# Optimization experiments

Measured on AMD Instinct MI355X. Metric: run time of the kernel, lower is better.

## Reference

```python
import jax, jax.numpy as jnp
import numpy as np
from math import pi

B, CIN, COUT, H, W, K, STRIDE, PAD = 4, 32, 64, 32, 32, 3, 1, 1


def setup_inputs() -> dict:
    key = jax.random.key(0)
    k1, k2, k3 = jax.random.split(key, 3)
    x = jax.random.normal(k1, (B, CIN, H, W), dtype=jnp.float32)
    probe = jax.random.uniform(k2, (1, CIN, COUT, 1, 1, K, K), dtype=jnp.float32, minval=-pi, maxval=pi)
    out_w = jax.random.uniform(k3, (1, CIN, COUT, 1, 1, K, K), dtype=jnp.float32, minval=-pi, maxval=pi)
    return {"x": x, "probe": probe, "out_w": out_w}


def _patches(x):
    # sliding-window gather, equivalent to x.unfold(2,K,S).unfold(3,K,S)
    p = jax.lax.conv_general_dilated_patches(
        x, filter_shape=(K, K), window_strides=(STRIDE, STRIDE),
        padding=[(PAD, PAD), (PAD, PAD)])  # (B, CIN*K*K, Ho, Wo), channel-major
    b, _, ho, wo = p.shape
    p = p.reshape(b, CIN, K, K, ho, wo)
    return jnp.transpose(p, (0, 1, 4, 5, 2, 3))  # (B, CIN, Ho, Wo, K, K)


def reference(x, probe, out_w):
    pat = _patches(x)[:, :, None]                 # (B, CIN, 1, Ho, Wo, K, K)
    act = jnp.cos(pat - probe) ** 3               # (B, CIN, COUT, Ho, Wo, K, K)
    cw = jnp.cos(out_w).reshape(CIN, COUT, K, K)  # squeeze broadcast dims
    sw = jnp.sin(out_w).reshape(CIN, COUT, K, K)
    out_x = jnp.einsum('cokl,bcohwkl->bohw', cw, act)
    out_y = jnp.einsum('cokl,bcohwkl->bohw', sw, act)
    return jnp.arctan2(out_y, out_x)              # (B, COUT, Ho, Wo)
```

## Files before the change

kernel.cpp:

```cpp
#include <hip/hip_runtime.h>
#include <math.h>


typedef _Float16 half8 __attribute__((ext_vector_type(8)));
typedef _Float16 half4 __attribute__((ext_vector_type(4)));
typedef float floatx4 __attribute__((ext_vector_type(4)));

#define B_TAP_STRIDE (16 * 128 * 16)
#define B_VSTRIDE (9u * 16 * 128 * 16)
#define FLAG_OFF (1u << 20)

#define AL_OFF 26112

#define BLOAD(dst, base)                     \
  do {                                       \
    dst##0 = *(const half8*)((base));        \
    dst##1 = *(const half8*)((base) + 8192); \
    dst##2 = *(const half8*)((base) + 16384);\
    dst##3 = *(const half8*)((base) + 24576);\
  } while (0)

__global__ __launch_bounds__(512, 2) void ring_fused(
    const float* __restrict__ x, const float* __restrict__ probe,
    const float* __restrict__ outw, char* __restrict__ Bg,
    float* __restrict__ out) {
  __shared__ __align__(16) char sA[52224];
  __shared__ float sEx[1024];

  int blk = blockIdx.x;
  int oh = blk & 1;
  int h = (blk >> 1) & 31;
  int b = blk >> 6;
  int tid = threadIdx.x;

  if (tid < 72) {
    int i = blk * 72 + tid;
    int q = i & 15;
    int n = (i >> 4) & 127;
    int tap = i >> 11;
    int o = n & 63;
    int xy = n >> 6;
    half8 hi, lo;
#pragma unroll
    for (int hf = 0; hf < 2; ++hf) {
      int c = q * 2 + hf;
      int idx = (c * 64 + o) * 9 + tap;
      float th = probe[idx];
      float wvv = outw[idx];
      float sth, cth, sw, cw;
      __sincosf(th, &sth, &cth);
      __sincosf(wvv, &sw, &cw);
      float c3 = cth * fmaf(4.0f * cth, cth, -3.0f);
      float s3 = sth * fmaf(-4.0f * sth, sth, 3.0f);
      float m = xy ? sw : cw;
      float v4[4] = {0.75f * m * cth, 0.75f * m * sth, 0.25f * m * c3,
                     0.25f * m * s3};
#pragma unroll
      for (int f = 0; f < 4; ++f) {
        _Float16 hv = (_Float16)v4[f];
        hi[hf * 4 + f] = hv;
        lo[hf * 4 + f] = (_Float16)((v4[f] - (float)hv) * 2048.0f);
      }
    }
    size_t off = (((size_t)tap * 16 + q) * 128 + n) * 16;
    *(half8*)(Bg + off) = hi;
    *(half8*)(Bg + off + B_VSTRIDE) = lo;
  }

  int lane = tid & 63;
  int wv = tid >> 6;
  int n16 = lane & 15;
  int quad = lane >> 4;
  int wt = wv >> 2;
  int xy = (wv >> 1) & 1;
  int og = wv & 1;

  {
    float xv[7];
#pragma unroll
    for (int it = 0; it < 7; ++it) {
      int u = tid + it * 512;
      int colidx = u % 34;
      int t = u / 34;
      int c = t & 31;
      int r = t >> 5;
      int hs = h + r - 1;
      int wsx = colidx - 1;
      bool valid = (u < 3264) && ((unsigned)hs < 32u) && ((unsigned)wsx < 32u);
      int xi = ((b * 32 + c) * 32 + ((unsigned)hs < 32u ? hs : 0)) * 32 +
               ((unsigned)wsx < 32u ? wsx : 0);
      xv[it] = valid ? x[xi] : 0.0f;
    }
#pragma unroll
    for (int it = 0; it < 7; ++it) {
      int u = tid + it * 512;
      if (u < 3264) {
        int colidx = u % 34;
        int t = u / 34;
        int c = t & 31;
        int r = t >> 5;
        int q = c >> 1;
        int hf = c & 1;
        int p = q ^ (colidx & 7);
        float s1, c1;
        __sincosf(xv[it], &s1, &c1);
        float c3 = c1 * fmaf(4.0f * c1, c1, -3.0f);
        float s3 = s1 * fmaf(-4.0f * s1, s1, 3.0f);
        float v4[4] = {c1, s1, c3, s3};
        half4 hi4, lo4;
#pragma unroll
        for (int f = 0; f < 4; ++f) {
          _Float16 hv = (_Float16)v4[f];
          hi4[f] = hv;
          lo4[f] = (_Float16)((v4[f] - (float)hv) * 2048.0f);
        }
        int ub = ((r * 34 + colidx) * 16 + p) * 16 + hf * 8;
        *(half4*)(sA + ub) = hi4;
        *(half4*)(sA + ub + AL_OFF) = lo4;
      }
    }
  }

  __syncthreads();
  unsigned int* flag = (unsigned int*)(Bg + FLAG_OFF);
  if (tid == 0) {
    __threadfence();
    atomicAdd(flag, 1u);
    while (atomicAdd(flag, 0u) < 256u) {
      __builtin_amdgcn_s_sleep(8);
    }
    __threadfence();
  }
  __syncthreads();

  int n_global = xy * 64 + oh * 32 + og * 16 + n16;
  const char* bLane = Bg + quad * 2048 + (size_t)n_global * 16;

  half8 BcH0, BcH1, BcH2, BcH3, BcL0, BcL1, BcL2, BcL3;
  half8 BnH0, BnH1, BnH2, BnH3, BnL0, BnL1, BnL2, BnL3;
  half8 BtH0, BtH1, BtH2, BtH3, BtL0, BtL1, BtL2, BtL3;
  BLOAD(BcH, bLane);
  BLOAD(BcL, bLane + B_VSTRIDE);
  BLOAD(BnH, bLane + B_TAP_STRIDE);
  BLOAD(BnL, bLane + B_TAP_STRIDE + B_VSTRIDE);

  floatx4 acc0 = {0.f, 0.f, 0.f, 0.f};
  floatx4 acc1 = {0.f, 0.f, 0.f, 0.f};
  floatx4 acc2 = {0.f, 0.f, 0.f, 0.f};

#pragma unroll
  for (int tap = 0; tap < 9; ++tap) {
    if (tap < 7) {
      const char* bt = bLane + (size_t)(tap + 2) * B_TAP_STRIDE;
      BLOAD(BtH, bt);
      BLOAD(BtL, bt + B_VSTRIDE);
    }

    int dk = tap / 3;
    int l = tap - dk * 3;
    int colidx = wt * 16 + n16 + l;
    int akey = colidx & 7;
    const char* aH = sA + (dk * 34 + colidx) * 256;
    const char* aL = aH + AL_OFF;

#pragma unroll
    for (int ks = 0; ks < 4; ++ks) {
      int pa = ((ks * 4 + quad) ^ akey) * 16;
      half8 Ah = *(const half8*)(aH + pa);
      half8 Al = *(const half8*)(aL + pa);
      half8 Bh = (ks == 0) ? BcH0 : (ks == 1) ? BcH1 : (ks == 2) ? BcH2 : BcH3;
      half8 Bl = (ks == 0) ? BcL0 : (ks == 1) ? BcL1 : (ks == 2) ? BcL2 : BcL3;
      acc0 = __builtin_amdgcn_mfma_f32_16x16x32_f16(Ah, Bh, acc0, 0, 0, 0);
      acc1 = __builtin_amdgcn_mfma_f32_16x16x32_f16(Al, Bh, acc1, 0, 0, 0);
      acc2 = __builtin_amdgcn_mfma_f32_16x16x32_f16(Ah, Bl, acc2, 0, 0, 0);
    }
    BcH0 = BnH0; BcH1 = BnH1; BcH2 = BnH2; BcH3 = BnH3;
    BcL0 = BnL0; BcL1 = BnL1; BcL2 = BnL2; BcL3 = BnL3;
    BnH0 = BtH0; BnH1 = BtH1; BnH2 = BtH2; BnH3 = BtH3;
    BnL0 = BtL0; BnL1 = BtL1; BnL2 = BtL2; BnL3 = BtL3;
  }

  floatx4 fin = acc0 + (acc1 + acc2) * (1.0f / 2048.0f);

  __syncthreads();
  if (xy == 1) {
#pragma unroll
    for (int r = 0; r < 4; ++r)
      sEx[((wt * 2 + og) * 16 + n16) * 16 + quad * 4 + r] = fin[r];
  }
  __syncthreads();
  if (xy == 0) {
    int o = oh * 32 + og * 16 + n16;
    float4 res;
    float* rp = (float*)&res;
#pragma unroll
    for (int r = 0; r < 4; ++r) {
      int m = quad * 4 + r;
      float ay = sEx[((wt * 2 + og) * 16 + n16) * 16 + m];
      rp[r] = atan2f(ay, fin[r]);
    }
    float* dst = out + (((size_t)(b * 64 + o) * 32 + h) * 32 + wt * 16 + quad * 4);
    *(float4*)dst = res;
  }
}

extern "C" void kernel_launch(void* const* d_in, const int* in_sizes, int n_in,
                              void* d_out, int out_size, void* d_ws, size_t ws_size,
                              hipStream_t stream) {
  const float* x = (const float*)d_in[0];
  const float* probe = (const float*)d_in[1];
  const float* outw = (const float*)d_in[2];
  char* Bg = (char*)d_ws;
  float* out = (float*)d_out;

  hipMemsetAsync(Bg + FLAG_OFF, 0, 4, stream);
  ring_fused<<<256, 512, 0, stream>>>(x, probe, outw, Bg, out);
}
```

Baseline: 80.06 us.

## Split weight prep into separate kernel and split K across waves

The weight-table preparation moves out of the fused kernel into its own small kernel, so the grid-wide atomic spin barrier and the flag memset go away. The main kernel now gives each wave half the channel chunks for both column tiles instead of all channels for one tile. Partial sums are reduced through shared memory before atan2. B-fragment register pressure is halved, so B loads can be issued before the A staging, but there is an extra launch and a heavier LDS reduction.

```diff
diff --git a/kernel.cpp b/kernel.cpp
--- a/kernel.cpp
+++ b/kernel.cpp
@@ -8,24 +8,56 @@
 
 #define B_TAP_STRIDE (16 * 128 * 16)
 #define B_VSTRIDE (9u * 16 * 128 * 16)
-#define FLAG_OFF (1u << 20)
 
 #define AL_OFF 26112
 
-#define BLOAD(dst, base)                     \
+__global__ __launch_bounds__(256) void ring_prep_b(
+    const float* __restrict__ probe, const float* __restrict__ outw,
+    char* __restrict__ Bg) {
+  int i = blockIdx.x * 256 + threadIdx.x;
+  int q = i & 15;
+  int n = (i >> 4) & 127;
+  int tap = i >> 11;
+  int o = n & 63;
+  int xy = n >> 6;
+  half8 hi, lo;
+#pragma unroll
+  for (int hf = 0; hf < 2; ++hf) {
+    int c = q * 2 + hf;
+    int idx = (c * 64 + o) * 9 + tap;
+    float th = probe[idx];
+    float wvv = outw[idx];
+    float sth, cth, sw, cw;
+    __sincosf(th, &sth, &cth);
+    __sincosf(wvv, &sw, &cw);
+    float c3 = cth * fmaf(4.0f * cth, cth, -3.0f);
+    float s3 = sth * fmaf(-4.0f * sth, sth, 3.0f);
+    float m = xy ? sw : cw;
+    float v4[4] = {0.75f * m * cth, 0.75f * m * sth, 0.25f * m * c3,
+                   0.25f * m * s3};
+#pragma unroll
+    for (int f = 0; f < 4; ++f) {
+      _Float16 hv = (_Float16)v4[f];
+      hi[hf * 4 + f] = hv;
+      lo[hf * 4 + f] = (_Float16)((v4[f] - (float)hv) * 2048.0f);
+    }
+  }
+  size_t off = (((size_t)tap * 16 + q) * 128 + n) * 16;
+  *(half8*)(Bg + off) = hi;
+  *(half8*)(Bg + off + B_VSTRIDE) = lo;
+}
+
+#define BLOAD2(dst, base)                    \
   do {                                       \
     dst##0 = *(const half8*)((base));        \
     dst##1 = *(const half8*)((base) + 8192); \
-    dst##2 = *(const half8*)((base) + 16384);\
-    dst##3 = *(const half8*)((base) + 24576);\
   } while (0)
 
-__global__ __launch_bounds__(512, 2) void ring_fused(
-    const float* __restrict__ x, const float* __restrict__ probe,
-    const float* __restrict__ outw, char* __restrict__ Bg,
+__global__ __launch_bounds__(512, 2) void ring_mfma(
+    const float* __restrict__ x, const char* __restrict__ Bg,
     float* __restrict__ out) {
   __shared__ __align__(16) char sA[52224];
-  __shared__ float sEx[1024];
+  __shared__ __align__(16) float sR[4096];
 
   int blk = blockIdx.x;
   int oh = blk & 1;
@@ -33,47 +65,24 @@
   int b = blk >> 6;
   int tid = threadIdx.x;
 
-  if (tid < 72) {
-    int i = blk * 72 + tid;
-    int q = i & 15;
-    int n = (i >> 4) & 127;
-    int tap = i >> 11;
-    int o = n & 63;
-    int xy = n >> 6;
-    half8 hi, lo;
-#pragma unroll
-    for (int hf = 0; hf < 2; ++hf) {
-      int c = q * 2 + hf;
-      int idx = (c * 64 + o) * 9 + tap;
-      float th = probe[idx];
-      float wvv = outw[idx];
-      float sth, cth, sw, cw;
-      __sincosf(th, &sth, &cth);
-      __sincosf(wvv, &sw, &cw);
-      float c3 = cth * fmaf(4.0f * cth, cth, -3.0f);
-      float s3 = sth * fmaf(-4.0f * sth, sth, 3.0f);
-      float m = xy ? sw : cw;
-      float v4[4] = {0.75f * m * cth, 0.75f * m * sth, 0.25f * m * c3,
-                     0.25f * m * s3};
-#pragma unroll
-      for (int f = 0; f < 4; ++f) {
-        _Float16 hv = (_Float16)v4[f];
-        hi[hf * 4 + f] = hv;
-        lo[hf * 4 + f] = (_Float16)((v4[f] - (float)hv) * 2048.0f);
-      }
-    }
-    size_t off = (((size_t)tap * 16 + q) * 128 + n) * 16;
-    *(half8*)(Bg + off) = hi;
-    *(half8*)(Bg + off + B_VSTRIDE) = lo;
-  }
-
   int lane = tid & 63;
   int wv = tid >> 6;
   int n16 = lane & 15;
   int quad = lane >> 4;
-  int wt = wv >> 2;
+  int kg = wv >> 2;
   int xy = (wv >> 1) & 1;
   int og = wv & 1;
+
+  int n_global = xy * 64 + oh * 32 + og * 16 + n16;
+  const char* bLane = Bg + (kg * 8 + quad) * 2048 + (size_t)n_global * 16;
+
+  half8 BcH0, BcH1, BcL0, BcL1;
+  half8 BnH0, BnH1, BnL0, BnL1;
+  half8 BtH0, BtH1, BtL0, BtL1;
+  BLOAD2(BcH, bLane);
+  BLOAD2(BcL, bLane + B_VSTRIDE);
+  BLOAD2(BnH, bLane + B_TAP_STRIDE);
+  BLOAD2(BnL, bLane + B_TAP_STRIDE + B_VSTRIDE);
 
   {
     float xv[7];
@@ -121,86 +130,77 @@
     }
   }
 
+  floatx4 acc0[2], acc1[2], acc2[2];
+#pragma unroll
+  for (int wt = 0; wt < 2; ++wt) {
+    acc0[wt] = (floatx4){0.f, 0.f, 0.f, 0.f};
+    acc1[wt] = (floatx4){0.f, 0.f, 0.f, 0.f};
+    acc2[wt] = (floatx4){0.f, 0.f, 0.f, 0.f};
+  }
+
   __syncthreads();
-  unsigned int* flag = (unsigned int*)(Bg + FLAG_OFF);
-  if (tid == 0) {
-    __threadfence();
-    atomicAdd(flag, 1u);
-    while (atomicAdd(flag, 0u) < 256u) {
-      __builtin_amdgcn_s_sleep(8);
-    }
-    __threadfence();
-  }
-  __syncthreads();
-
-  int n_global = xy * 64 + oh * 32 + og * 16 + n16;
-  const char* bLane = Bg + quad * 2048 + (size_t)n_global * 16;
-
-  half8 BcH0, BcH1, BcH2, BcH3, BcL0, BcL1, BcL2, BcL3;
-  half8 BnH0, BnH1, BnH2, BnH3, BnL0, BnL1, BnL2, BnL3;
-  half8 BtH0, BtH1, BtH2, BtH3, BtL0, BtL1, BtL2, BtL3;
-  BLOAD(BcH, bLane);
-  BLOAD(BcL, bLane + B_VSTRIDE);
-  BLOAD(BnH, bLane + B_TAP_STRIDE);
-  BLOAD(BnL, bLane + B_TAP_STRIDE + B_VSTRIDE);
-
-  floatx4 acc0 = {0.f, 0.f, 0.f, 0.f};
-  floatx4 acc1 = {0.f, 0.f, 0.f, 0.f};
-  floatx4 acc2 = {0.f, 0.f, 0.f, 0.f};
 
 #pragma unroll
   for (int tap = 0; tap < 9; ++tap) {
     if (tap < 7) {
       const char* bt = bLane + (size_t)(tap + 2) * B_TAP_STRIDE;
-      BLOAD(BtH, bt);
-      BLOAD(BtL, bt + B_VSTRIDE);
+      BLOAD2(BtH, bt);
+      BLOAD2(BtL, bt + B_VSTRIDE);
     }
 
     int dk = tap / 3;
     int l = tap - dk * 3;
-    int colidx = wt * 16 + n16 + l;
-    int akey = colidx & 7;
-    const char* aH = sA + (dk * 34 + colidx) * 256;
-    const char* aL = aH + AL_OFF;
-
-#pragma unroll
-    for (int ks = 0; ks < 4; ++ks) {
-      int pa = ((ks * 4 + quad) ^ akey) * 16;
-      half8 Ah = *(const half8*)(aH + pa);
-      half8 Al = *(const half8*)(aL + pa);
-      half8 Bh = (ks == 0) ? BcH0 : (ks == 1) ? BcH1 : (ks == 2) ? BcH2 : BcH3;
-      half8 Bl = (ks == 0) ? BcL0 : (ks == 1) ? BcL1 : (ks == 2) ? BcL2 : BcL3;
-      acc0 = __builtin_amdgcn_mfma_f32_16x16x32_f16(Ah, Bh, acc0, 0, 0, 0);
-      acc1 = __builtin_amdgcn_mfma_f32_16x16x32_f16(Al, Bh, acc1, 0, 0, 0);
-      acc2 = __builtin_amdgcn_mfma_f32_16x16x32_f16(Ah, Bl, acc2, 0, 0, 0);
-    }
-    BcH0 = BnH0; BcH1 = BnH1; BcH2 = BnH2; BcH3 = BnH3;
-    BcL0 = BnL0; BcL1 = BnL1; BcL2 = BnL2; BcL3 = BnL3;
-    BnH0 = BtH0; BnH1 = BtH1; BnH2 = BtH2; BnH3 = BtH3;
-    BnL0 = BtL0; BnL1 = BtL1; BnL2 = BtL2; BnL3 = BtL3;
-  }
-
-  floatx4 fin = acc0 + (acc1 + acc2) * (1.0f / 2048.0f);
-
+#pragma unroll
+    for (int wt = 0; wt < 2; ++wt) {
+      int colidx = wt * 16 + n16 + l;
+      int akey = colidx & 7;
+      const char* aH = sA + (dk * 34 + colidx) * 256;
+      const char* aL = aH + AL_OFF;
+#pragma unroll
+      for (int ksl = 0; ksl < 2; ++ksl) {
+        int chunk = (kg * 2 + ksl) * 4 + quad;
+        int pa = (chunk ^ akey) * 16;
+        half8 Ah = *(const half8*)(aH + pa);
+        half8 Al = *(const half8*)(aL + pa);
+        half8 Bh = ksl ? BcH1 : BcH0;
+        half8 Bl = ksl ? BcL1 : BcL0;
+        acc0[wt] = __builtin_amdgcn_mfma_f32_16x16x32_f16(Ah, Bh, acc0[wt], 0, 0, 0);
+        acc1[wt] = __builtin_amdgcn_mfma_f32_16x16x32_f16(Al, Bh, acc1[wt], 0, 0, 0);
+        acc2[wt] = __builtin_amdgcn_mfma_f32_16x16x32_f16(Ah, Bl, acc2[wt], 0, 0, 0);
+      }
+    }
+    BcH0 = BnH0; BcH1 = BnH1; BcL0 = BnL0; BcL1 = BnL1;
+    BnH0 = BtH0; BnH1 = BtH1; BnL0 = BtL0; BnL1 = BtL1;
+  }
+
+  floatx4 finA = acc0[0] + (acc1[0] + acc2[0]) * (1.0f / 2048.0f);
+  floatx4 finB = acc0[1] + (acc1[1] + acc2[1]) * (1.0f / 2048.0f);
+
+  if (wv >= 2) {
+    int basei = wv * 512 + n16 * 16 + quad * 4;
+    *(floatx4*)(sR + basei) = finA;
+    *(floatx4*)(sR + basei + 256) = finB;
+  }
   __syncthreads();
-  if (xy == 1) {
-#pragma unroll
-    for (int r = 0; r < 4; ++r)
-      sEx[((wt * 2 + og) * 16 + n16) * 16 + quad * 4 + r] = fin[r];
-  }
-  __syncthreads();
-  if (xy == 0) {
+  if (wv < 2) {
     int o = oh * 32 + og * 16 + n16;
-    float4 res;
-    float* rp = (float*)&res;
-#pragma unroll
-    for (int r = 0; r < 4; ++r) {
-      int m = quad * 4 + r;
-      float ay = sEx[((wt * 2 + og) * 16 + n16) * 16 + m];
-      rp[r] = atan2f(ay, fin[r]);
-    }
-    float* dst = out + (((size_t)(b * 64 + o) * 32 + h) * 32 + wt * 16 + quad * 4);
-    *(float4*)dst = res;
+#pragma unroll
+    for (int wt = 0; wt < 2; ++wt) {
+      floatx4 fin = wt ? finB : finA;
+      int sb = wt * 256 + n16 * 16 + quad * 4;
+      floatx4 axE = *(const floatx4*)(sR + (4 + og) * 512 + sb);
+      floatx4 ay1 = *(const floatx4*)(sR + (2 + og) * 512 + sb);
+      floatx4 ay2 = *(const floatx4*)(sR + (6 + og) * 512 + sb);
+      floatx4 ax4 = fin + axE;
+      floatx4 ay4 = ay1 + ay2;
+      float4 res;
+      float* rp = (float*)&res;
+#pragma unroll
+      for (int r = 0; r < 4; ++r) rp[r] = atan2f(ay4[r], ax4[r]);
+      float* dst =
+          out + (((size_t)(b * 64 + o) * 32 + h) * 32 + wt * 16 + quad * 4);
+      *(float4*)dst = res;
+    }
   }
 }
 
@@ -213,6 +213,6 @@
   char* Bg = (char*)d_ws;
   float* out = (float*)d_out;
 
-  hipMemsetAsync(Bg + FLAG_OFF, 0, 4, stream);
-  ring_fused<<<256, 512, 0, stream>>>(x, probe, outw, Bg, out);
+  ring_prep_b<<<72, 256, 0, stream>>>(probe, outw, Bg);
+  ring_mfma<<<256, 512, 0, stream>>>(x, Bg, out);
 }
```

New measurement: 66.87 us. 1.2x faster.
